# Performance work log

Hardware: AMD Instinct MI355X
Metric: run time of the kernel (lower is better)

## Reference

```python
import jax, jax.numpy as jnp
import numpy as np

B, T, D = 2, 2048, 4096
H, KH, HD = 32, 8, 128          # n_heads, n_kv_heads, head_dim = D // H
WINDOW, NGLOBAL = 1024, 32      # sliding window size, global sink tokens
ROPE_BASE = 500000.0


def _rope_tables(seq_len, dim):
    inv_freq = 1.0 / (ROPE_BASE ** (np.arange(0, dim, 2, dtype=np.float64) / dim))
    freqs = np.outer(np.arange(seq_len, dtype=np.float64), inv_freq)
    emb = np.concatenate([freqs, freqs], axis=-1)  # [T, HD]
    cos = jnp.asarray(np.cos(emb), dtype=jnp.float32)[None, None]  # [1,1,T,HD]
    sin = jnp.asarray(np.sin(emb), dtype=jnp.float32)[None, None]
    return cos, sin


def _window_global_mask(seq_len, window, n_global):
    i = np.arange(seq_len)[:, None]  # query pos
    j = np.arange(seq_len)[None, :]  # key pos
    causal = j <= i
    local = j > (i - window)
    global_keys = j < n_global
    return jnp.asarray(causal & (local | global_keys))[None, None]  # [1,1,T,T] bool


def rotate_half(x):
    x1, x2 = jnp.split(x, 2, axis=-1)
    return jnp.concatenate([-x2, x1], axis=-1)


def setup_inputs() -> dict:
    key = jax.random.key(0)
    kx, kq, kk, kv, ko = jax.random.split(key, 5)
    s = 1.0 / np.sqrt(D)
    x = jax.random.normal(kx, (B, T, D), dtype=jnp.float32)
    # Linear weights stored [in, out] (y = x @ W), same math as torch's x @ W.T
    Wq = jax.random.normal(kq, (D, H * HD), dtype=jnp.float32) * s
    Wk = jax.random.normal(kk, (D, KH * HD), dtype=jnp.float32) * s
    Wv = jax.random.normal(kv, (D, KH * HD), dtype=jnp.float32) * s
    Wo = jax.random.normal(ko, (H * HD, D), dtype=jnp.float32) * s
    cos, sin = _rope_tables(T, HD)
    mask = _window_global_mask(T, WINDOW, NGLOBAL)
    return {"x": x, "Wq": Wq, "Wk": Wk, "Wv": Wv, "Wo": Wo,
            "cos": cos, "sin": sin, "mask": mask}


def reference(x, Wq, Wk, Wv, Wo, cos, sin, mask):
    Bx, Tx, Dx = x.shape
    q = (x @ Wq).reshape(Bx, Tx, H, HD).transpose(0, 2, 1, 3)   # [B,H,T,HD]
    k = (x @ Wk).reshape(Bx, Tx, KH, HD).transpose(0, 2, 1, 3)  # [B,KH,T,HD]
    v = (x @ Wv).reshape(Bx, Tx, KH, HD).transpose(0, 2, 1, 3)
    # RoPE
    q = q * cos + rotate_half(q) * sin
    k = k * cos + rotate_half(k) * sin
    # GQA: repeat_interleave KV heads to match query heads (faithful to source)
    factor = H // KH
    k = jnp.repeat(k, factor, axis=1)  # [B,H,T,HD]
    v = jnp.repeat(v, factor, axis=1)
    # SDPA with dense bool mask (True = attend), default scale 1/sqrt(HD)
    scale = 1.0 / np.sqrt(HD)
    scores = jnp.einsum('bhqd,bhkd->bhqk', q, k) * scale  # [B,H,T,T]
    scores = jnp.where(mask, scores, jnp.finfo(scores.dtype).min)
    attn = jax.nn.softmax(scores, axis=-1)
    out = jnp.einsum('bhqk,bhkd->bhqd', attn, v)
    out = out.transpose(0, 2, 1, 3).reshape(Bx, Tx, H * HD)
    return out @ Wo
```

## Files before the change

kernel.cpp:

```cpp
#include <hip/hip_runtime.h>
#include <stdint.h>

typedef unsigned short u16;
typedef __bf16 bf16x8 __attribute__((ext_vector_type(8)));
typedef float f32x4 __attribute__((ext_vector_type(4)));

#define D_MODEL 4096
#define T_SEQ   2048
#define B_SZ    2
#define NH      32
#define NKV     8
#define HDIM    128
#define WINDOW  1024
#define NGLOB   32
#define QSTR    6144

static constexpr float SCALE = 0.08838834764831845f;

__device__ __forceinline__ u16 f2b(float f) {
  __bf16 h = (__bf16)f;
  return __builtin_bit_cast(u16, h);
}

__global__ __launch_bounds__(256) void convert_bf16_kernel(const float* __restrict__ in,
                                                           u16* __restrict__ outp, int n4) {
  int i = blockIdx.x * 256 + threadIdx.x;
  if (i >= n4) return;
  float4 v = ((const float4*)in)[i];
  ushort4 o;
  o.x = f2b(v.x); o.y = f2b(v.y); o.z = f2b(v.z); o.w = f2b(v.w);
  ((ushort4*)outp)[i] = o;
}

__global__ __launch_bounds__(256) void transpose_w_kernel(const float* __restrict__ W,
                                                          u16* __restrict__ Wt, int Kd, int Nd) {
  __shared__ float tile[32][33];
  int tx = threadIdx.x & 31, ty = threadIdx.x >> 5;
  int bx = blockIdx.x * 32;
  int by = blockIdx.y * 32;
#pragma unroll
  for (int i = 0; i < 4; ++i)
    tile[ty + i * 8][tx] = W[(size_t)(by + ty + i * 8) * Nd + bx + tx];
  __syncthreads();
#pragma unroll
  for (int i = 0; i < 4; ++i)
    Wt[(size_t)(bx + ty + i * 8) * Kd + by + tx] = f2b(tile[tx][ty + i * 8]);
}

__global__ __launch_bounds__(256) void transpose_v_kernel(const u16* __restrict__ in,
                                                          u16* __restrict__ outp) {
  __shared__ u16 tile[32][33];
  int tx = threadIdx.x & 31, ty = threadIdx.x >> 5;
  int x0 = blockIdx.x * 32;
  int t0 = blockIdx.y * 32;
  int b = blockIdx.z;
  const u16* src = in + (size_t)b * T_SEQ * QSTR;
  u16* dst = outp + (size_t)b * (NKV * HDIM) * T_SEQ;
#pragma unroll
  for (int i = 0; i < 4; ++i)
    tile[ty + i * 8][tx] = src[(size_t)(t0 + ty + i * 8) * QSTR + x0 + tx];
  __syncthreads();
#pragma unroll
  for (int i = 0; i < 4; ++i)
    dst[(size_t)(x0 + ty + i * 8) * T_SEQ + t0 + tx] = tile[tx][ty + i * 8];
}

template <typename CT>
__global__ __launch_bounds__(512, 2) void gemm256_kernel(const u16* __restrict__ A,
                                                         const u16* __restrict__ Bt,
                                                         CT* __restrict__ C,
                                                         int ldc, int K) {
  __shared__ u16 sh[65536];
  const int tid = threadIdx.x;
  const int wave = tid >> 6, lane = tid & 63;
  const int g = lane >> 4, li = lane & 15;
  const int wr = wave >> 2, wc = wave & 3;
  const int m0 = blockIdx.y * 256, n0 = blockIdx.x * 256;
  const int r0 = tid >> 3;
  const int cs = ((tid & 7) ^ ((tid >> 3) & 7)) << 3;
  const u16* pA = A + (size_t)(m0 + r0) * K + cs;
  const u16* pB = Bt + (size_t)(n0 + r0) * K + cs;
  const int sl0 = (g ^ (li & 7)) << 3;
  const int sl1 = ((4 + g) ^ (li & 7)) << 3;
  const int nT = K >> 6;

  f32x4 acc[8][4];
  f32x4 zz = {0.f, 0.f, 0.f, 0.f};
#pragma unroll
  for (int M = 0; M < 8; ++M)
#pragma unroll
    for (int n = 0; n < 4; ++n) acc[M][n] = zz;

  auto stage = [&](const u16* src0, int ts, int dstBase) {
#pragma unroll
    for (int i = 0; i < 2; ++i) {
      const u16* s = src0 + (size_t)(i * 64) * K + ts * 64;
      __builtin_amdgcn_global_load_lds((__attribute__((address_space(1))) void*)s,
                                       (__attribute__((address_space(3))) void*)(sh + dstBase + i * 4096 + wave * 512),
                                       16, 0, 0);
    }
  };

  stage(pA, 0, 0);
  stage(pA + (size_t)128 * K, 0, 8192);
  stage(pB, 0, 16384);
  stage(pB + (size_t)128 * K, 0, 24576);
  stage(pB, 1, 32768 + 16384);
  stage(pB + (size_t)128 * K, 1, 32768 + 24576);
  stage(pA, 1, 32768);
  asm volatile("s_waitcnt vmcnt(6)" ::: "memory");
  __builtin_amdgcn_s_barrier();

  bf16x8 afr[4][2], bfr[4][2];
  for (int t = 0; t < nT; ++t) {
    const int cur = t & 1;
    const int ab = cur * 32768, bb = ab + 16384;
    const int nb = (cur ^ 1) * 32768;
    const int tn1 = (t + 1 < nT) ? t + 1 : nT - 1;
    const int tn2 = (t + 2 < nT) ? t + 2 : nT - 1;
#pragma unroll
    for (int n = 0; n < 4; ++n) {
      int row = wc * 64 + n * 16 + li;
      bfr[n][0] = *(const bf16x8*)&sh[bb + row * 64 + sl0];
      bfr[n][1] = *(const bf16x8*)&sh[bb + row * 64 + sl1];
    }
#pragma unroll
    for (int m = 0; m < 4; ++m) {
      int row = wr * 128 + m * 16 + li;
      afr[m][0] = *(const bf16x8*)&sh[ab + row * 64 + sl0];
      afr[m][1] = *(const bf16x8*)&sh[ab + row * 64 + sl1];
    }
    stage(pA + (size_t)128 * K, tn1, nb + 8192);
    __builtin_amdgcn_s_barrier();
    asm volatile("s_waitcnt lgkmcnt(0)" ::: "memory");
    __builtin_amdgcn_sched_barrier(0);
    __builtin_amdgcn_s_setprio(1);
#pragma unroll
    for (int m = 0; m < 4; ++m)
#pragma unroll
      for (int n = 0; n < 2; ++n) {
        acc[m][n] = __builtin_amdgcn_mfma_f32_16x16x32_bf16(afr[m][0], bfr[n][0], acc[m][n], 0, 0, 0);
        acc[m][n] = __builtin_amdgcn_mfma_f32_16x16x32_bf16(afr[m][1], bfr[n][1], acc[m][n], 0, 0, 0);
      }
    __builtin_amdgcn_s_setprio(0);
    __builtin_amdgcn_s_barrier();
    stage(pB, tn2, bb);
    __builtin_amdgcn_s_barrier();
    __builtin_amdgcn_s_setprio(1);
#pragma unroll
    for (int m = 0; m < 4; ++m)
#pragma unroll
      for (int n = 2; n < 4; ++n) {
        acc[m][n] = __builtin_amdgcn_mfma_f32_16x16x32_bf16(afr[m][0], bfr[n][0], acc[m][n], 0, 0, 0);
        acc[m][n] = __builtin_amdgcn_mfma_f32_16x16x32_bf16(afr[m][1], bfr[n][1], acc[m][n], 0, 0, 0);
      }
    __builtin_amdgcn_s_setprio(0);
    __builtin_amdgcn_s_barrier();
#pragma unroll
    for (int m = 0; m < 4; ++m) {
      int row = wr * 128 + 64 + m * 16 + li;
      afr[m][0] = *(const bf16x8*)&sh[ab + row * 64 + sl0];
      afr[m][1] = *(const bf16x8*)&sh[ab + row * 64 + sl1];
    }
    stage(pB + (size_t)128 * K, tn2, bb + 8192);
    __builtin_amdgcn_s_barrier();
    asm volatile("s_waitcnt lgkmcnt(0)" ::: "memory");
    __builtin_amdgcn_sched_barrier(0);
    __builtin_amdgcn_s_setprio(1);
#pragma unroll
    for (int m = 0; m < 4; ++m)
#pragma unroll
      for (int n = 0; n < 2; ++n) {
        acc[4 + m][n] = __builtin_amdgcn_mfma_f32_16x16x32_bf16(afr[m][0], bfr[n][0], acc[4 + m][n], 0, 0, 0);
        acc[4 + m][n] = __builtin_amdgcn_mfma_f32_16x16x32_bf16(afr[m][1], bfr[n][1], acc[4 + m][n], 0, 0, 0);
      }
    __builtin_amdgcn_s_setprio(0);
    __builtin_amdgcn_s_barrier();
    stage(pA, tn2, ab);
    __builtin_amdgcn_s_barrier();
    __builtin_amdgcn_s_setprio(1);
#pragma unroll
    for (int m = 0; m < 4; ++m)
#pragma unroll
      for (int n = 2; n < 4; ++n) {
        acc[4 + m][n] = __builtin_amdgcn_mfma_f32_16x16x32_bf16(afr[m][0], bfr[n][0], acc[4 + m][n], 0, 0, 0);
        acc[4 + m][n] = __builtin_amdgcn_mfma_f32_16x16x32_bf16(afr[m][1], bfr[n][1], acc[4 + m][n], 0, 0, 0);
      }
    __builtin_amdgcn_s_setprio(0);
    asm volatile("s_waitcnt vmcnt(6)" ::: "memory");
    __builtin_amdgcn_s_barrier();
  }
#pragma unroll
  for (int M = 0; M < 8; ++M)
#pragma unroll
    for (int n = 0; n < 4; ++n)
#pragma unroll
      for (int r = 0; r < 4; ++r) {
        int row = m0 + wr * 128 + M * 16 + g * 4 + r;
        int col = n0 + wc * 64 + n * 16 + li;
        if constexpr (sizeof(CT) == 2)
          C[(size_t)row * ldc + col] = (CT)f2b(acc[M][n][r]);
        else
          C[(size_t)row * ldc + col] = acc[M][n][r];
      }
}

__global__ __launch_bounds__(512, 2) void gemm192_kernel(const u16* __restrict__ A,
                                                         const u16* __restrict__ Bt,
                                                         u16* __restrict__ C,
                                                         int ldc, int K) {
  __shared__ u16 sh[57344];
  const int tid = threadIdx.x;
  const int wave = tid >> 6, lane = tid & 63;
  const int g = lane >> 4, li = lane & 15;
  const int wr = wave >> 2, wc = wave & 3;
  const int m0 = blockIdx.y * 256, n0 = blockIdx.x * 192;
  const int r0 = tid >> 3;
  const int cs = ((tid & 7) ^ ((tid >> 3) & 7)) << 3;
  const u16* pA = A + (size_t)(m0 + r0) * K + cs;
  const u16* pB = Bt + (size_t)(n0 + r0) * K + cs;
  const int sl0 = (g ^ (li & 7)) << 3;
  const int sl1 = ((4 + g) ^ (li & 7)) << 3;
  const int nT = K >> 6;

  f32x4 acc[8][3];
  f32x4 zz = {0.f, 0.f, 0.f, 0.f};
#pragma unroll
  for (int M = 0; M < 8; ++M)
#pragma unroll
    for (int n = 0; n < 3; ++n) acc[M][n] = zz;

  auto stage64 = [&](const u16* src0, int ts, int dstU16) {
    __builtin_amdgcn_global_load_lds(
        (__attribute__((address_space(1))) void*)(src0 + (size_t)ts * 64),
        (__attribute__((address_space(3))) void*)(sh + dstU16 + wave * 512), 16, 0, 0);
  };

#pragma unroll
  for (int u = 0; u < 4; ++u) stage64(pA + (size_t)(u * 64) * K, 0, u * 4096);
#pragma unroll
  for (int u = 0; u < 3; ++u) stage64(pB + (size_t)(u * 64) * K, 0, 16384 + u * 4096);
#pragma unroll
  for (int u = 0; u < 4; ++u) stage64(pA + (size_t)(u * 64) * K, 1, 28672 + u * 4096);
#pragma unroll
  for (int u = 0; u < 3; ++u) stage64(pB + (size_t)(u * 64) * K, 1, 28672 + 16384 + u * 4096);
  asm volatile("s_waitcnt vmcnt(7)" ::: "memory");
  __builtin_amdgcn_s_barrier();

  bf16x8 afr[4][2], bfr[3][2];
  for (int t = 0; t < nT; ++t) {
    const int ab = (t & 1) * 28672, bb = ab + 16384;
    const int tn2 = (t + 2 < nT) ? t + 2 : nT - 1;
#pragma unroll
    for (int n = 0; n < 3; ++n) {
      int row = wc * 48 + n * 16 + li;
      bfr[n][0] = *(const bf16x8*)&sh[bb + row * 64 + sl0];
      bfr[n][1] = *(const bf16x8*)&sh[bb + row * 64 + sl1];
    }
#pragma unroll
    for (int m = 0; m < 4; ++m) {
      int row = wr * 128 + m * 16 + li;
      afr[m][0] = *(const bf16x8*)&sh[ab + row * 64 + sl0];
      afr[m][1] = *(const bf16x8*)&sh[ab + row * 64 + sl1];
    }
    __builtin_amdgcn_s_barrier();
    asm volatile("s_waitcnt lgkmcnt(0)" ::: "memory");
    __builtin_amdgcn_sched_barrier(0);
    __builtin_amdgcn_s_setprio(1);
#pragma unroll
    for (int m = 0; m < 4; ++m)
#pragma unroll
      for (int n = 0; n < 2; ++n) {
        acc[m][n] = __builtin_amdgcn_mfma_f32_16x16x32_bf16(afr[m][0], bfr[n][0], acc[m][n], 0, 0, 0);
        acc[m][n] = __builtin_amdgcn_mfma_f32_16x16x32_bf16(afr[m][1], bfr[n][1], acc[m][n], 0, 0, 0);
      }
    __builtin_amdgcn_s_setprio(0);
    __builtin_amdgcn_s_barrier();
    stage64(pB, tn2, bb);
    stage64(pB + (size_t)64 * K, tn2, bb + 4096);
    stage64(pA, tn2, ab);
    __builtin_amdgcn_s_barrier();
    __builtin_amdgcn_s_setprio(1);
#pragma unroll
    for (int m = 0; m < 4; ++m) {
      acc[m][2] = __builtin_amdgcn_mfma_f32_16x16x32_bf16(afr[m][0], bfr[2][0], acc[m][2], 0, 0, 0);
      acc[m][2] = __builtin_amdgcn_mfma_f32_16x16x32_bf16(afr[m][1], bfr[2][1], acc[m][2], 0, 0, 0);
    }
    __builtin_amdgcn_s_setprio(0);
    __builtin_amdgcn_s_barrier();
#pragma unroll
    for (int m = 0; m < 4; ++m) {
      int row = wr * 128 + 64 + m * 16 + li;
      afr[m][0] = *(const bf16x8*)&sh[ab + row * 64 + sl0];
      afr[m][1] = *(const bf16x8*)&sh[ab + row * 64 + sl1];
    }
    stage64(pB + (size_t)128 * K, tn2, bb + 8192);
    stage64(pA + (size_t)128 * K, tn2, ab + 8192);
    __builtin_amdgcn_s_barrier();
    asm volatile("s_waitcnt lgkmcnt(0)" ::: "memory");
    __builtin_amdgcn_sched_barrier(0);
    __builtin_amdgcn_s_setprio(1);
#pragma unroll
    for (int m = 0; m < 4; ++m)
#pragma unroll
      for (int n = 0; n < 2; ++n) {
        acc[4 + m][n] = __builtin_amdgcn_mfma_f32_16x16x32_bf16(afr[m][0], bfr[n][0], acc[4 + m][n], 0, 0, 0);
        acc[4 + m][n] = __builtin_amdgcn_mfma_f32_16x16x32_bf16(afr[m][1], bfr[n][1], acc[4 + m][n], 0, 0, 0);
      }
    __builtin_amdgcn_s_setprio(0);
    __builtin_amdgcn_s_barrier();
    stage64(pA + (size_t)64 * K, tn2, ab + 4096);
    stage64(pA + (size_t)192 * K, tn2, ab + 12288);
    __builtin_amdgcn_s_barrier();
    __builtin_amdgcn_s_setprio(1);
#pragma unroll
    for (int m = 0; m < 4; ++m) {
      acc[4 + m][2] = __builtin_amdgcn_mfma_f32_16x16x32_bf16(afr[m][0], bfr[2][0], acc[4 + m][2], 0, 0, 0);
      acc[4 + m][2] = __builtin_amdgcn_mfma_f32_16x16x32_bf16(afr[m][1], bfr[2][1], acc[4 + m][2], 0, 0, 0);
    }
    __builtin_amdgcn_s_setprio(0);
    asm volatile("s_waitcnt vmcnt(7)" ::: "memory");
    __builtin_amdgcn_s_barrier();
  }
#pragma unroll
  for (int M = 0; M < 8; ++M)
#pragma unroll
    for (int n = 0; n < 3; ++n)
#pragma unroll
      for (int r = 0; r < 4; ++r) {
        int row = m0 + wr * 128 + M * 16 + g * 4 + r;
        int col = n0 + wc * 48 + n * 16 + li;
        C[(size_t)row * ldc + col] = f2b(acc[M][n][r]);
      }
}

__global__ __launch_bounds__(256) void rope_kernel(u16* __restrict__ qkv,
                                                   const float* __restrict__ cosp,
                                                   const float* __restrict__ sinp) {
  int idx = blockIdx.x * 256 + threadIdx.x;
  int d8 = idx & 7;
  int rest = idx >> 3;
  int hh = rest % (NH + NKV);
  int bt = rest / (NH + NKV);
  if (bt >= B_SZ * T_SEQ) return;
  int tok = bt & (T_SEQ - 1);
  int d0 = d8 * 8;
  const float4* cp = (const float4*)(cosp + (size_t)tok * HDIM + d0);
  const float4* sp = (const float4*)(sinp + (size_t)tok * HDIM + d0);
  float4 cA = cp[0], cB = cp[1];
  float4 sA = sp[0], sB = sp[1];
  float cc[8] = {cA.x, cA.y, cA.z, cA.w, cB.x, cB.y, cB.z, cB.w};
  float ss[8] = {sA.x, sA.y, sA.z, sA.w, sB.x, sB.y, sB.z, sB.w};
  float scl = (hh < NH) ? SCALE : 1.0f;
  u16* base = qkv + (size_t)bt * QSTR + hh * HDIM;
  bf16x8 v1 = *(const bf16x8*)(base + d0);
  bf16x8 v2 = *(const bf16x8*)(base + d0 + 64);
  bf16x8 o1, o2;
#pragma unroll
  for (int j = 0; j < 8; ++j) {
    float xa = (float)v1[j], xb = (float)v2[j];
    o1[j] = (__bf16)((xa * cc[j] - xb * ss[j]) * scl);
    o2[j] = (__bf16)((xb * cc[j] + xa * ss[j]) * scl);
  }
  *(bf16x8*)(base + d0) = o1;
  *(bf16x8*)(base + d0 + 64) = o2;
}

__global__ __launch_bounds__(512) void attn_kernel(const u16* __restrict__ qp,
                                                   const u16* __restrict__ kp,
                                                   const u16* __restrict__ vtp,
                                                   u16* __restrict__ ctx) {
  __shared__ u16 Kt[64 * 128];
  __shared__ u16 Vt[128 * 64];
  __shared__ u16 Pl[8][16 * 64];
  int tid = threadIdx.x;
  int w = tid >> 6, lane = tid & 63;
  int g = lane >> 4, li = lane & 15;
  int i0 = blockIdx.x * 128;
  int h = blockIdx.y, b = blockIdx.z;
  int kh = h >> 2;
  f32x4 zz = {0.f, 0.f, 0.f, 0.f};

  bf16x8 qf[4];
  size_t qrow = (size_t)(b * T_SEQ + i0 + w * 16 + li) * QSTR + h * HDIM;
#pragma unroll
  for (int c = 0; c < 4; ++c) qf[c] = *(const bf16x8*)(qp + qrow + c * 32 + g * 8);

  f32x4 o[8];
#pragma unroll
  for (int f = 0; f < 8; ++f) o[f] = zz;
  float m_s = -1e30f, l_s = 0.f;
  const int irow = i0 + w * 16 + li;

  int jmax = i0 + 127;
  for (int j0 = 0; j0 <= jmax; j0 += 64) {
    if (!((j0 < NGLOB) || (j0 + 63 > i0 - WINDOW))) continue;
    __syncthreads();
#pragma unroll
    for (int i = 0; i < 2; ++i) {
      int o8 = tid + 512 * i;
      int krow = o8 >> 4, kch = o8 & 15;
      size_t gk = (size_t)(b * T_SEQ + j0 + krow) * QSTR + kh * HDIM + (kch ^ (krow & 7)) * 8;
      __builtin_amdgcn_global_load_lds((__attribute__((address_space(1))) void*)(kp + gk),
                                       (__attribute__((address_space(3))) void*)(Kt + o8 * 8),
                                       16, 0, 0);
      int vrow = o8 >> 3, vch = o8 & 7;
      size_t gv = ((size_t)(b * NKV + kh) * HDIM + vrow) * T_SEQ + j0 + (vch ^ (vrow & 7)) * 8;
      __builtin_amdgcn_global_load_lds((__attribute__((address_space(1))) void*)(vtp + gv),
                                       (__attribute__((address_space(3))) void*)(Vt + o8 * 8),
                                       16, 0, 0);
    }
    __syncthreads();

    f32x4 s[4];
#pragma unroll
    for (int kb = 0; kb < 4; ++kb) s[kb] = zz;
#pragma unroll
    for (int c = 0; c < 4; ++c) {
      int hd0 = c * 32 + g * 8;
#pragma unroll
      for (int kb = 0; kb < 4; ++kb) {
        int key = kb * 16 + li;
        bf16x8 kf = *(const bf16x8*)&Kt[(key * 128 + hd0) ^ ((key & 7) << 3)];
        s[kb] = __builtin_amdgcn_mfma_f32_16x16x32_bf16(kf, qf[c], s[kb], 0, 0, 0);
      }
    }

    float x[4][4];
    float mt = -1e30f;
#pragma unroll
    for (int kb = 0; kb < 4; ++kb)
#pragma unroll
      for (int r = 0; r < 4; ++r) {
        int j = j0 + kb * 16 + g * 4 + r;
        bool vm = (j <= irow) && ((j > irow - WINDOW) || (j < NGLOB));
        float xx = vm ? s[kb][r] : -1e30f;
        x[kb][r] = xx;
        mt = fmaxf(mt, xx);
      }
    mt = fmaxf(mt, __shfl_xor(mt, 16, 64));
    mt = fmaxf(mt, __shfl_xor(mt, 32, 64));
    float mn = fmaxf(m_s, mt);
    float corr = __expf(m_s - mn);
    m_s = mn;
    float rs = 0.f;
#pragma unroll
    for (int kb = 0; kb < 4; ++kb) {
      ushort4 pk;
#pragma unroll
      for (int r = 0; r < 4; ++r) {
        float p = __expf(x[kb][r] - mn);
        rs += p;
        ((u16*)&pk)[r] = f2b(p);
      }
      *(ushort4*)&Pl[w][(li * 64 + kb * 16 + g * 4) ^ ((li & 7) << 3)] = pk;
    }
    rs += __shfl_xor(rs, 16, 64);
    rs += __shfl_xor(rs, 32, 64);
    l_s = l_s * corr + rs;

    float c4[4];
#pragma unroll
    for (int r = 0; r < 4; ++r) c4[r] = __shfl(corr, g * 4 + r, 16);
#pragma unroll
    for (int f = 0; f < 8; ++f) {
      o[f][0] *= c4[0]; o[f][1] *= c4[1];
      o[f][2] *= c4[2]; o[f][3] *= c4[3];
    }

    bf16x8 pa0 = *(const bf16x8*)&Pl[w][(li * 64 + 0 + g * 8) ^ ((li & 7) << 3)];
    bf16x8 pa1 = *(const bf16x8*)&Pl[w][(li * 64 + 32 + g * 8) ^ ((li & 7) << 3)];

#pragma unroll
    for (int f = 0; f < 8; ++f) {
      int hd = f * 16 + li;
      bf16x8 v0 = *(const bf16x8*)&Vt[(hd * 64 + 0 + g * 8) ^ ((li & 7) << 3)];
      bf16x8 v1 = *(const bf16x8*)&Vt[(hd * 64 + 32 + g * 8) ^ ((li & 7) << 3)];
      o[f] = __builtin_amdgcn_mfma_f32_16x16x32_bf16(pa0, v0, o[f], 0, 0, 0);
      o[f] = __builtin_amdgcn_mfma_f32_16x16x32_bf16(pa1, v1, o[f], 0, 0, 0);
    }
  }

  float l4[4];
#pragma unroll
  for (int r = 0; r < 4; ++r) l4[r] = __shfl(l_s, g * 4 + r, 16);
#pragma unroll
  for (int f = 0; f < 8; ++f)
#pragma unroll
    for (int r = 0; r < 4; ++r) {
      size_t orow = (size_t)(b * T_SEQ + i0 + w * 16 + g * 4 + r) * (NH * HDIM) + h * HDIM + f * 16 + li;
      ctx[orow] = f2b(o[f][r] / l4[r]);
    }
}

extern "C" void kernel_launch(void* const* d_in, const int* in_sizes, int n_in,
                              void* d_out, int out_size, void* d_ws, size_t ws_size,
                              hipStream_t stream) {
  const float* x    = (const float*)d_in[0];
  const float* Wq   = (const float*)d_in[1];
  const float* Wk   = (const float*)d_in[2];
  const float* Wv   = (const float*)d_in[3];
  const float* Wo   = (const float*)d_in[4];
  const float* cosp = (const float*)d_in[5];
  const float* sinp = (const float*)d_in[6];

  char* ws = (char*)d_ws;
  u16* xb     = (u16*)(ws + 0ull);
  u16* Wqkvt  = (u16*)(ws + 33554432ull);
  u16* Wot    = (u16*)(ws + 83886080ull);
  u16* qkv    = (u16*)(ws + 117440512ull);
  u16* ctx    = xb;
  u16* vT     = Wqkvt;

  convert_bf16_kernel<<<16384, 256, 0, stream>>>(x, xb, 4194304);
  transpose_w_kernel<<<dim3(128, 128), 256, 0, stream>>>(Wq, Wqkvt, 4096, 4096);
  transpose_w_kernel<<<dim3(32, 128), 256, 0, stream>>>(Wk, Wqkvt + (size_t)4096 * 4096, 4096, 1024);
  transpose_w_kernel<<<dim3(32, 128), 256, 0, stream>>>(Wv, Wqkvt + (size_t)5120 * 4096, 4096, 1024);
  transpose_w_kernel<<<dim3(128, 128), 256, 0, stream>>>(Wo, Wot, 4096, 4096);

  gemm192_kernel<<<dim3(32, 16), 512, 0, stream>>>(xb, Wqkvt, qkv, QSTR, 4096);

  transpose_v_kernel<<<dim3(32, 64, 2), 256, 0, stream>>>(qkv + 5120, vT);

  rope_kernel<<<5120, 256, 0, stream>>>(qkv, cosp, sinp);

  attn_kernel<<<dim3(16, 32, 2), 512, 0, stream>>>(qkv, qkv + 4096, vT, ctx);

  gemm256_kernel<float><<<dim3(16, 16), 512, 0, stream>>>(ctx, Wot, (float*)d_out, 4096, 4096);
}
```

Measured before the change: 553.4 us.

## Double-buffer K/V tiles in attention and iterate only over visible tiles

The attention kernel now keeps two LDS buffers for K and V and issues the async global-to-LDS loads for the next key tile before computing on the current one, replacing the two barriers per tile with one wait and barrier at the end. The tile loop also computes its start and count directly from the sliding window plus a single global-sink tile, instead of scanning every tile and skipping masked ones. This aims to hide global load latency behind MFMA work and drop empty loop iterations. The cost is double the K/V LDS footprint, which may lower occupancy, plus more complex index logic.

```diff
diff --git a/kernel.cpp b/kernel.cpp
--- a/kernel.cpp
+++ b/kernel.cpp
@@ -370,8 +370,8 @@
                                                    const u16* __restrict__ kp,
                                                    const u16* __restrict__ vtp,
                                                    u16* __restrict__ ctx) {
-  __shared__ u16 Kt[64 * 128];
-  __shared__ u16 Vt[128 * 64];
+  __shared__ u16 Kt[2][64 * 128];
+  __shared__ u16 Vt[2][128 * 64];
   __shared__ u16 Pl[8][16 * 64];
   int tid = threadIdx.x;
   int w = tid >> 6, lane = tid & 63;
@@ -392,25 +392,38 @@
   float m_s = -1e30f, l_s = 0.f;
   const int irow = i0 + w * 16 + li;
 
-  int jmax = i0 + 127;
-  for (int j0 = 0; j0 <= jmax; j0 += 64) {
-    if (!((j0 < NGLOB) || (j0 + 63 > i0 - WINDOW))) continue;
-    __syncthreads();
+  const int jlo = (i0 > WINDOW) ? (i0 - WINDOW) : 0;
+  const int nglob = (jlo > 0) ? 1 : 0;
+  const int ntiles = nglob + (i0 + 64 - jlo) / 64 + 1;
+
+  auto j_of = [&](int t) { return (nglob && t == 0) ? 0 : jlo + (t - nglob) * 64; };
+
+  auto stage = [&](int t, int buf) {
+    int j0 = j_of(t);
 #pragma unroll
     for (int i = 0; i < 2; ++i) {
       int o8 = tid + 512 * i;
       int krow = o8 >> 4, kch = o8 & 15;
       size_t gk = (size_t)(b * T_SEQ + j0 + krow) * QSTR + kh * HDIM + (kch ^ (krow & 7)) * 8;
       __builtin_amdgcn_global_load_lds((__attribute__((address_space(1))) void*)(kp + gk),
-                                       (__attribute__((address_space(3))) void*)(Kt + o8 * 8),
+                                       (__attribute__((address_space(3))) void*)(Kt[buf] + o8 * 8),
                                        16, 0, 0);
       int vrow = o8 >> 3, vch = o8 & 7;
       size_t gv = ((size_t)(b * NKV + kh) * HDIM + vrow) * T_SEQ + j0 + (vch ^ (vrow & 7)) * 8;
       __builtin_amdgcn_global_load_lds((__attribute__((address_space(1))) void*)(vtp + gv),
-                                       (__attribute__((address_space(3))) void*)(Vt + o8 * 8),
+                                       (__attribute__((address_space(3))) void*)(Vt[buf] + o8 * 8),
                                        16, 0, 0);
     }
-    __syncthreads();
+  };
+
+  stage(0, 0);
+  asm volatile("s_waitcnt vmcnt(0)" ::: "memory");
+  __builtin_amdgcn_s_barrier();
+
+  for (int t = 0; t < ntiles; ++t) {
+    const int buf = t & 1;
+    const int j0 = j_of(t);
+    if (t + 1 < ntiles) stage(t + 1, buf ^ 1);
 
     f32x4 s[4];
 #pragma unroll
@@ -421,7 +434,7 @@
 #pragma unroll
       for (int kb = 0; kb < 4; ++kb) {
         int key = kb * 16 + li;
-        bf16x8 kf = *(const bf16x8*)&Kt[(key * 128 + hd0) ^ ((key & 7) << 3)];
+        bf16x8 kf = *(const bf16x8*)&Kt[buf][(key * 128 + hd0) ^ ((key & 7) << 3)];
         s[kb] = __builtin_amdgcn_mfma_f32_16x16x32_bf16(kf, qf[c], s[kb], 0, 0, 0);
       }
     }
@@ -474,11 +487,14 @@
 #pragma unroll
     for (int f = 0; f < 8; ++f) {
       int hd = f * 16 + li;
-      bf16x8 v0 = *(const bf16x8*)&Vt[(hd * 64 + 0 + g * 8) ^ ((li & 7) << 3)];
-      bf16x8 v1 = *(const bf16x8*)&Vt[(hd * 64 + 32 + g * 8) ^ ((li & 7) << 3)];
+      bf16x8 v0 = *(const bf16x8*)&Vt[buf][(hd * 64 + 0 + g * 8) ^ ((li & 7) << 3)];
+      bf16x8 v1 = *(const bf16x8*)&Vt[buf][(hd * 64 + 32 + g * 8) ^ ((li & 7) << 3)];
       o[f] = __builtin_amdgcn_mfma_f32_16x16x32_bf16(pa0, v0, o[f], 0, 0, 0);
       o[f] = __builtin_amdgcn_mfma_f32_16x16x32_bf16(pa1, v1, o[f], 0, 0, 0);
     }
+
+    asm volatile("s_waitcnt vmcnt(0)" ::: "memory");
+    __builtin_amdgcn_s_barrier();
   }
 
   float l4[4];
```

Result: no change. 558.1 us (+0.8%).
